# Kernel tuning notes

Hardware: AMD Instinct MI355X
Metric: run time of the kernel (lower is better)

## Reference

```python
import jax, jax.numpy as jnp
import numpy as np

N_NODES = 100000
N_EDGES = 1600000
IN_DIM = 128
HID = 128


def sage_conv(x, src, dst, W_l, W_r, b, num_nodes):
    # PyG SAGEConv (mean aggregation): out = lin_l(mean_{j in N(i)} x_j) + lin_r(x_i)
    msgs = x[src]                                            # [E, F] gather
    agg = jax.ops.segment_sum(msgs, dst, num_segments=num_nodes)  # [N, F]
    cnt = jax.ops.segment_sum(jnp.ones((src.shape[0],), x.dtype), dst,
                              num_segments=num_nodes)        # [N]
    agg = agg / jnp.maximum(cnt, 1.0)[:, None]               # mean; 0 for isolated nodes
    return agg @ W_l + b + x @ W_r


def setup_inputs() -> dict:
    key = jax.random.key(0)
    ks = jax.random.split(key, 12)
    s_in = 1.0 / np.sqrt(IN_DIM)
    s_h = 1.0 / np.sqrt(HID)
    return {
        "x": jax.random.normal(ks[0], (N_NODES, IN_DIM), jnp.float32),
        "edge_index": jax.random.randint(ks[1], (2, N_EDGES), 0, N_NODES, jnp.int64),
        "Wl1": jax.random.normal(ks[2], (IN_DIM, HID), jnp.float32) * s_in,
        "Wr1": jax.random.normal(ks[3], (IN_DIM, HID), jnp.float32) * s_in,
        "b1": jnp.zeros((HID,), jnp.float32),
        "Wl2": jax.random.normal(ks[4], (HID, HID), jnp.float32) * s_h,
        "Wr2": jax.random.normal(ks[5], (HID, HID), jnp.float32) * s_h,
        "b2": jnp.zeros((HID,), jnp.float32),
        "Wp": jax.random.normal(ks[6], (HID, 1), jnp.float32) * s_h,
        "bp": jnp.zeros((1,), jnp.float32),
        "Wd": jax.random.normal(ks[7], (HID, 1), jnp.float32) * s_h,
        "bd": jnp.zeros((1,), jnp.float32),
    }


def reference(x, edge_index, Wl1, Wr1, b1, Wl2, Wr2, b2, Wp, bp, Wd, bd):
    src, dst = edge_index[0], edge_index[1]
    h = jax.nn.relu(sage_conv(x, src, dst, Wl1, Wr1, b1, N_NODES))
    h = jax.nn.relu(sage_conv(h, src, dst, Wl2, Wr2, b2, N_NODES))
    preds = h @ Wp + bp                      # [N, 1]
    diffs = jax.nn.sigmoid(h @ Wd + bd)      # [N, 1]
    return (preds - diffs, preds + diffs)
```

## Files before the change

### kernel.cpp

```cpp
#include <hip/hip_runtime.h>
#include <hip/hip_bf16.h>

#define N_NODES 100000
#define N_EDGES 1600000
#define NBUCK 1563
#define BCAP 1216
#define PADC 1408
#define ACHUNK 4096
#define GTILES 1563
#define PABLK 391

typedef __bf16 bf16x8 __attribute__((ext_vector_type(8)));
typedef __bf16 bf16x4 __attribute__((ext_vector_type(4)));
typedef float  f32x4  __attribute__((ext_vector_type(4)));
typedef float  f32x2  __attribute__((ext_vector_type(2)));


#define ACC16(v)                                             \
  a01 += __builtin_amdgcn_cvt_pk_f32_fp8((v).x, false);      \
  a23 += __builtin_amdgcn_cvt_pk_f32_fp8((v).x, true);       \
  a45 += __builtin_amdgcn_cvt_pk_f32_fp8((v).y, false);      \
  a67 += __builtin_amdgcn_cvt_pk_f32_fp8((v).y, true);       \
  a89 += __builtin_amdgcn_cvt_pk_f32_fp8((v).z, false);      \
  aAB += __builtin_amdgcn_cvt_pk_f32_fp8((v).z, true);       \
  aCD += __builtin_amdgcn_cvt_pk_f32_fp8((v).w, false);      \
  aEF += __builtin_amdgcn_cvt_pk_f32_fp8((v).w, true);

#define WFRAG(ct, c) (*(const bf16x8*)&Wswz[(size_t)((((w * 4 + (ct)) * 4 + (c)) * 64) + lane) * 8])


__global__ __launch_bounds__(256) void init_kernel(int* __restrict__ bcnt,
                                                   int* __restrict__ P1s,
                                                   int* __restrict__ P2s,
                                                   const float* __restrict__ Wl1,
                                                   const float* __restrict__ Wr1,
                                                   const float* __restrict__ Wl2,
                                                   const float* __restrict__ Wr2,
                                                   __bf16* __restrict__ W1out,
                                                   __bf16* __restrict__ W2out) {
  const int b = blockIdx.x, t = threadIdx.x;
  if (b == 0) {
    for (int i = t; i < NBUCK; i += 256) bcnt[i] = 0;
    if (t < 32) { P1s[t] = 0; P2s[t] = 0; }
    return;
  }
  int gi = (b - 1) * 256 + t;
  bool L2 = gi >= 32768;
  int i = gi & 32767;
  int j = i & 7;
  int lane = (i >> 3) & 63;
  int c = (i >> 9) & 3;
  int tile = i >> 11;
  int k = c * 32 + ((lane >> 4) * 8) + j;
  int krow = L2 ? (((k & 7) << 4) | (k >> 3)) : k;
  int col = tile * 16 + (lane & 15);
  const float* Wl = L2 ? Wl2 : Wl1;
  const float* Wr = L2 ? Wr2 : Wr1;
  float v = (col < 128) ? Wl[krow * 128 + col] : Wr[krow * 128 + (col - 128)];
  (L2 ? W2out : W1out)[i] = (__bf16)v;
}


__global__ __launch_bounds__(256, 4) void work1_kernel(
    const float* __restrict__ A, const __bf16* __restrict__ Wswz,
    const float* __restrict__ bias, unsigned char* __restrict__ P,
    __bf16* __restrict__ R, int M,
    const int* __restrict__ src, const int* __restrict__ dst,
    int* __restrict__ bcnt, unsigned* __restrict__ packed, int E) {
  __shared__ __align__(16) char smem[64 * 144 * 2];
  const int t = threadIdx.x;

  if (blockIdx.x < PABLK) {
    int* hist = (int*)smem;
    int* curs = (int*)(smem + 6272);
    for (int i = t; i < NBUCK; i += 256) hist[i] = 0;
    __syncthreads();

    const int base = blockIdx.x * ACHUNK;
    const int lim = min(base + ACHUNK, E);

    int dloc[16], sloc[16];
    int myn = 0;
    for (int i = base + t; i < lim; i += 256) {
      dloc[myn] = dst[i];
      sloc[myn] = src[i];
      ++myn;
    }
    for (int k = 0; k < myn; ++k) atomicAdd(&hist[dloc[k] >> 6], 1);
    __syncthreads();

    for (int i = t; i < NBUCK; i += 256) {
      int h = hist[i];
      curs[i] = (h > 0) ? atomicAdd(&bcnt[i], h) : 0;
    }
    __syncthreads();

    for (int k = 0; k < myn; ++k) {
      int d = dloc[k];
      int b = d >> 6;
      int pos = atomicAdd(&curs[b], 1);
      if (pos < BCAP)
        packed[(size_t)b * BCAP + pos] = ((unsigned)sloc[k] << 6) | (unsigned)(d & 63);
    }
    return;
  }

  __bf16 (*ldsA)[144] = (__bf16 (*)[144])smem;
  const int lane = t & 63;
  const int w = t >> 6;
  const int q = lane >> 4;
  const int s = lane & 15;
  const int m0 = (blockIdx.x - PABLK) * 64;

#pragma unroll
  for (int it = 0; it < 8; ++it) {
    int row = it * 8 + (t >> 5);
    int col = (t & 31) * 4;
    float4 v = make_float4(0.f, 0.f, 0.f, 0.f);
    if (m0 + row < M) v = *(const float4*)&A[(size_t)(m0 + row) * 128 + col];
    bf16x4 bv;
    bv.x = (__bf16)v.x; bv.y = (__bf16)v.y; bv.z = (__bf16)v.z; bv.w = (__bf16)v.w;
    *(bf16x4*)&ldsA[row][col] = bv;
  }

  float breg[4];
#pragma unroll
  for (int j = 0; j < 4; ++j)
    breg[j] = (w >= 2) ? bias[((w - 2) * 4 + j) * 16 + s] : 0.f;

  __syncthreads();

#pragma unroll
  for (int half = 0; half < 2; ++half) {
    f32x4 acc[8];
    f32x4 zero = {0.f, 0.f, 0.f, 0.f};
#pragma unroll
    for (int i = 0; i < 8; ++i) acc[i] = zero;

    bf16x8 b0 = WFRAG(0, 0), b1 = WFRAG(1, 0), b2 = WFRAG(2, 0), b3 = WFRAG(3, 0);
#pragma unroll
    for (int c = 0; c < 4; ++c) {
      bf16x8 n0, n1, n2, n3;
      if (c < 3) { n0 = WFRAG(0, c + 1); n1 = WFRAG(1, c + 1); n2 = WFRAG(2, c + 1); n3 = WFRAG(3, c + 1); }
      bf16x8 a0 = *(const bf16x8*)&ldsA[(half * 2 + 0) * 16 + s][c * 32 + q * 8];
      bf16x8 a1 = *(const bf16x8*)&ldsA[(half * 2 + 1) * 16 + s][c * 32 + q * 8];
      acc[0] = __builtin_amdgcn_mfma_f32_16x16x32_bf16(a0, b0, acc[0], 0, 0, 0);
      acc[4] = __builtin_amdgcn_mfma_f32_16x16x32_bf16(a1, b0, acc[4], 0, 0, 0);
      acc[1] = __builtin_amdgcn_mfma_f32_16x16x32_bf16(a0, b1, acc[1], 0, 0, 0);
      acc[5] = __builtin_amdgcn_mfma_f32_16x16x32_bf16(a1, b1, acc[5], 0, 0, 0);
      acc[2] = __builtin_amdgcn_mfma_f32_16x16x32_bf16(a0, b2, acc[2], 0, 0, 0);
      acc[6] = __builtin_amdgcn_mfma_f32_16x16x32_bf16(a1, b2, acc[6], 0, 0, 0);
      acc[3] = __builtin_amdgcn_mfma_f32_16x16x32_bf16(a0, b3, acc[3], 0, 0, 0);
      acc[7] = __builtin_amdgcn_mfma_f32_16x16x32_bf16(a1, b3, acc[7], 0, 0, 0);
      if (c < 3) { b0 = n0; b1 = n1; b2 = n2; b3 = n3; }
    }

#pragma unroll
    for (int i = 0; i < 2; ++i) {
      int rt = half * 2 + i;
#pragma unroll
      for (int r = 0; r < 4; ++r) {
        int row = m0 + rt * 16 + q * 4 + r;
        if (row < M) {
          if (w < 2) {
            unsigned v = 0;
            v = __builtin_amdgcn_cvt_pk_fp8_f32(acc[i * 4 + 0][r], acc[i * 4 + 1][r], v, false);
            v = __builtin_amdgcn_cvt_pk_fp8_f32(acc[i * 4 + 2][r], acc[i * 4 + 3][r], v, true);
            *(unsigned*)&P[(size_t)row * 128 + s * 8 + w * 4] = v;
          } else {
            bf16x4 o;
#pragma unroll
            for (int ct = 0; ct < 4; ++ct) o[ct] = (__bf16)(acc[i * 4 + ct][r] + breg[ct]);
            *(bf16x4*)&R[(size_t)row * 128 + s * 8 + (w - 2) * 4] = o;
          }
        }
      }
    }
  }
}


__global__ __launch_bounds__(256, 4) void fusedB_kernel(
    const unsigned char* __restrict__ P1, __bf16* R,
    const unsigned* __restrict__ pck, const int* __restrict__ bcnt,
    const __bf16* __restrict__ Wswz, const float* __restrict__ bias,
    unsigned char* __restrict__ P2, int* __restrict__ srt,
    int* __restrict__ meta, int N) {
  __shared__ __bf16 Hlds[64][144];
  __shared__ int ssrcL[PADC];
  __shared__ int hist[64], pexcl[64], curs[64], scanb[64];
  __shared__ int gsteal;
  const int t = threadIdx.x;
  const int lane = t & 63;
  const int w = t >> 6;
  const int q = lane >> 4;
  const int s = lane & 15;
  const int b = blockIdx.x, nb = b * 64;

  if (t < 64) hist[t] = 0;
  if (t == 0) gsteal = 0;
  __syncthreads();

  const int ecnt = min(bcnt[b], BCAP);
  const unsigned* pk = pck + (size_t)b * BCAP;
  unsigned ploc[5];
  int myn = 0;
  for (int i = t; i < ecnt; i += 256) {
    unsigned p = pk[i];
    ploc[myn++] = p;
    atomicAdd(&hist[p & 63u], 1);
  }
  __syncthreads();

  int c0 = (t < 64) ? hist[t] : 0;
  int pc = (c0 + 3) & ~3;
  int x = pc;
  if (t < 64) scanb[t] = x;
  __syncthreads();
  for (int d = 1; d < 64; d <<= 1) {
    int y = (t >= d && t < 64) ? scanb[t - d] : 0;
    __syncthreads();
    if (t < 64) { x += y; scanb[t] = x; }
    __syncthreads();
  }
  if (t < 64) { pexcl[t] = x - pc; curs[t] = x - pc; }
  __syncthreads();

  for (int k = 0; k < myn; ++k) {
    unsigned p = ploc[k];
    int r = atomicAdd(&curs[p & 63u], 1);
    ssrcL[r] = (int)(p >> 6);
  }
  if (t < 64)
    for (int j = c0; j < pc; ++j) ssrcL[pexcl[t] + j] = N;
  __syncthreads();

  for (int i = t; i < PADC; i += 256) srt[(size_t)b * PADC + i] = ssrcL[i];
  if (t < 64) meta[b * 64 + t] = (pexcl[t] << 16) | hist[t];

  const int s8 = lane & 7;
  const int g8 = lane >> 3;
  const unsigned char* Pb = P1 + (size_t)s8 * 16;
  for (;;) {
    int n8;
    if (lane == 0) n8 = atomicAdd(&gsteal, 8);
    n8 = __shfl(n8, 0, 64);
    if (n8 >= 64) break;
    int dl = n8 + g8;
    int node = nb + dl;
    int start = pexcl[dl];
    int dg = hist[dl];
    int pend = start + ((dg + 3) & ~3);

    f32x2 a01 = {0.f, 0.f}, a23 = {0.f, 0.f}, a45 = {0.f, 0.f}, a67 = {0.f, 0.f};
    f32x2 a89 = {0.f, 0.f}, aAB = {0.f, 0.f}, aCD = {0.f, 0.f}, aEF = {0.f, 0.f};
    int cur = start;
    for (; cur + 8 <= pend; cur += 8) {
      int4 sv0 = *(const int4*)&ssrcL[cur];
      int4 sv1 = *(const int4*)&ssrcL[cur + 4];
      uint4 v0 = *(const uint4*)(Pb + (size_t)sv0.x * 128);
      uint4 v1 = *(const uint4*)(Pb + (size_t)sv0.y * 128);
      uint4 v2 = *(const uint4*)(Pb + (size_t)sv0.z * 128);
      uint4 v3 = *(const uint4*)(Pb + (size_t)sv0.w * 128);
      uint4 v4 = *(const uint4*)(Pb + (size_t)sv1.x * 128);
      uint4 v5 = *(const uint4*)(Pb + (size_t)sv1.y * 128);
      uint4 v6 = *(const uint4*)(Pb + (size_t)sv1.z * 128);
      uint4 v7 = *(const uint4*)(Pb + (size_t)sv1.w * 128);
      ACC16(v0) ACC16(v1) ACC16(v2) ACC16(v3)
      ACC16(v4) ACC16(v5) ACC16(v6) ACC16(v7)
    }
    if (cur < pend) {
      int4 sv = *(const int4*)&ssrcL[cur];
      uint4 v0 = *(const uint4*)(Pb + (size_t)sv.x * 128);
      uint4 v1 = *(const uint4*)(Pb + (size_t)sv.y * 128);
      uint4 v2 = *(const uint4*)(Pb + (size_t)sv.z * 128);
      uint4 v3 = *(const uint4*)(Pb + (size_t)sv.w * 128);
      ACC16(v0) ACC16(v1) ACC16(v2) ACC16(v3)
    }

    int nc = min(node, N - 1);
    float inv = 1.0f / (float)(dg > 0 ? dg : 1);
    const int p16 = s8 * 16;
    bf16x8 rv0 = *(const bf16x8*)&R[(size_t)nc * 128 + p16];
    bf16x8 rv1 = *(const bf16x8*)&R[(size_t)nc * 128 + p16 + 8];
    float ac[16] = {a01[0], a01[1], a23[0], a23[1], a45[0], a45[1], a67[0], a67[1],
                    a89[0], a89[1], aAB[0], aAB[1], aCD[0], aCD[1], aEF[0], aEF[1]};
    bf16x8 h0, h1;
#pragma unroll
    for (int j = 0; j < 8; ++j) {
      h0[j] = (__bf16)fmaxf(ac[j] * inv + (float)rv0[j], 0.f);
      h1[j] = (__bf16)fmaxf(ac[8 + j] * inv + (float)rv1[j], 0.f);
    }
    *(bf16x8*)&Hlds[dl][p16] = h0;
    *(bf16x8*)&Hlds[dl][p16 + 8] = h1;
  }
  __syncthreads();

  float breg[4];
#pragma unroll
  for (int j = 0; j < 4; ++j)
    breg[j] = (w >= 2) ? bias[((w - 2) * 4 + j) * 16 + s] : 0.f;

#pragma unroll
  for (int half = 0; half < 2; ++half) {
    f32x4 acc[8];
    f32x4 zero = {0.f, 0.f, 0.f, 0.f};
#pragma unroll
    for (int i = 0; i < 8; ++i) acc[i] = zero;

#pragma unroll
    for (int c = 0; c < 4; ++c) {
      bf16x8 a0 = *(const bf16x8*)&Hlds[(half * 2 + 0) * 16 + s][c * 32 + q * 8];
      bf16x8 a1 = *(const bf16x8*)&Hlds[(half * 2 + 1) * 16 + s][c * 32 + q * 8];
#pragma unroll
      for (int ct = 0; ct < 4; ++ct) {
        bf16x8 b = *(const bf16x8*)&Wswz[(size_t)((((w * 4 + ct) * 4 + c) * 64) + lane) * 8];
        acc[ct]     = __builtin_amdgcn_mfma_f32_16x16x32_bf16(a0, b, acc[ct], 0, 0, 0);
        acc[4 + ct] = __builtin_amdgcn_mfma_f32_16x16x32_bf16(a1, b, acc[4 + ct], 0, 0, 0);
      }
    }

#pragma unroll
    for (int i = 0; i < 2; ++i) {
      int rt = half * 2 + i;
#pragma unroll
      for (int r = 0; r < 4; ++r) {
        int row = nb + rt * 16 + q * 4 + r;
        if (row < N) {
          if (w < 2) {
            unsigned v = 0;
            v = __builtin_amdgcn_cvt_pk_fp8_f32(acc[i * 4 + 0][r], acc[i * 4 + 1][r], v, false);
            v = __builtin_amdgcn_cvt_pk_fp8_f32(acc[i * 4 + 2][r], acc[i * 4 + 3][r], v, true);
            *(unsigned*)&P2[(size_t)row * 128 + s * 8 + w * 4] = v;
          } else {
            bf16x4 o;
#pragma unroll
            for (int ct = 0; ct < 4; ++ct) o[ct] = (__bf16)(acc[i * 4 + ct][r] + breg[ct]);
            *(bf16x4*)&R[(size_t)row * 128 + s * 8 + (w - 2) * 4] = o;
          }
        }
      }
    }
  }
}


__global__ __launch_bounds__(256, 4) void fusedC_kernel(
    const unsigned char* __restrict__ P2, const __bf16* __restrict__ R,
    const int* __restrict__ srt, const int* __restrict__ meta,
    float* __restrict__ out,
    const float* __restrict__ Wp, const float* __restrict__ Wd,
    const float* __restrict__ bp, const float* __restrict__ bd, int N) {
  __shared__ int ssrcL[PADC];
  __shared__ int hist[64], pexcl[64];
  __shared__ int gsteal;
  const int t = threadIdx.x;
  const int lane = t & 63;
  const int b = blockIdx.x, nb = b * 64;

  for (int i = t; i < PADC; i += 256) ssrcL[i] = srt[(size_t)b * PADC + i];
  if (t < 64) {
    int m = meta[b * 64 + t];
    pexcl[t] = m >> 16;
    hist[t] = m & 0xffff;
  }
  if (t == 0) gsteal = 0;
  __syncthreads();

  const int s8 = lane & 7;
  const int g8 = lane >> 3;
  const unsigned char* Pb = P2 + (size_t)s8 * 16;
  for (;;) {
    int n8;
    if (lane == 0) n8 = atomicAdd(&gsteal, 8);
    n8 = __shfl(n8, 0, 64);
    if (n8 >= 64) break;
    int dl = n8 + g8;
    int node = nb + dl;
    int start = pexcl[dl];
    int dg = hist[dl];
    int pend = start + ((dg + 3) & ~3);

    f32x2 a01 = {0.f, 0.f}, a23 = {0.f, 0.f}, a45 = {0.f, 0.f}, a67 = {0.f, 0.f};
    f32x2 a89 = {0.f, 0.f}, aAB = {0.f, 0.f}, aCD = {0.f, 0.f}, aEF = {0.f, 0.f};
    int cur = start;
    for (; cur + 8 <= pend; cur += 8) {
      int4 sv0 = *(const int4*)&ssrcL[cur];
      int4 sv1 = *(const int4*)&ssrcL[cur + 4];
      uint4 v0 = *(const uint4*)(Pb + (size_t)sv0.x * 128);
      uint4 v1 = *(const uint4*)(Pb + (size_t)sv0.y * 128);
      uint4 v2 = *(const uint4*)(Pb + (size_t)sv0.z * 128);
      uint4 v3 = *(const uint4*)(Pb + (size_t)sv0.w * 128);
      uint4 v4 = *(const uint4*)(Pb + (size_t)sv1.x * 128);
      uint4 v5 = *(const uint4*)(Pb + (size_t)sv1.y * 128);
      uint4 v6 = *(const uint4*)(Pb + (size_t)sv1.z * 128);
      uint4 v7 = *(const uint4*)(Pb + (size_t)sv1.w * 128);
      ACC16(v0) ACC16(v1) ACC16(v2) ACC16(v3)
      ACC16(v4) ACC16(v5) ACC16(v6) ACC16(v7)
    }
    if (cur < pend) {
      int4 sv = *(const int4*)&ssrcL[cur];
      uint4 v0 = *(const uint4*)(Pb + (size_t)sv.x * 128);
      uint4 v1 = *(const uint4*)(Pb + (size_t)sv.y * 128);
      uint4 v2 = *(const uint4*)(Pb + (size_t)sv.z * 128);
      uint4 v3 = *(const uint4*)(Pb + (size_t)sv.w * 128);
      ACC16(v0) ACC16(v1) ACC16(v2) ACC16(v3)
    }

    int nc = min(node, N - 1);
    float inv = 1.0f / (float)(dg > 0 ? dg : 1);
    const int p16 = s8 * 16;
    bf16x8 rv0 = *(const bf16x8*)&R[(size_t)nc * 128 + p16];
    bf16x8 rv1 = *(const bf16x8*)&R[(size_t)nc * 128 + p16 + 8];
    float ac[16] = {a01[0], a01[1], a23[0], a23[1], a45[0], a45[1], a67[0], a67[1],
                    a89[0], a89[1], aAB[0], aAB[1], aCD[0], aCD[1], aEF[0], aEF[1]};
    float p = 0.f, dd = 0.f;
#pragma unroll
    for (int j = 0; j < 16; ++j) {
      int pos = p16 + j;
      int f = ((pos & 7) << 4) | (pos >> 3);
      float rvj = (float)((j < 8) ? rv0[j] : rv1[j - 8]);
      float h = fmaxf(ac[j] * inv + rvj, 0.f);
      p += h * Wp[f];
      dd += h * Wd[f];
    }
    p += __shfl_xor(p, 1, 64);  p += __shfl_xor(p, 2, 64);  p += __shfl_xor(p, 4, 64);
    dd += __shfl_xor(dd, 1, 64); dd += __shfl_xor(dd, 2, 64); dd += __shfl_xor(dd, 4, 64);
    if (node < N && s8 == 0) {
      float preds = p + bp[0];
      float sg = 1.0f / (1.0f + __expf(-(dd + bd[0])));
      out[node] = preds - sg;
      out[N + node] = preds + sg;
    }
  }
}


extern "C" void kernel_launch(void* const* d_in, const int* in_sizes, int n_in,
                              void* d_out, int out_size, void* d_ws, size_t ws_size,
                              hipStream_t stream) {
  const float* x    = (const float*)d_in[0];
  const int*   ei   = (const int*)d_in[1];
  const float* Wl1 = (const float*)d_in[2];
  const float* Wr1 = (const float*)d_in[3];
  const float* b1  = (const float*)d_in[4];
  const float* Wl2 = (const float*)d_in[5];
  const float* Wr2 = (const float*)d_in[6];
  const float* b2  = (const float*)d_in[7];
  const float* Wp  = (const float*)d_in[8];
  const float* bp  = (const float*)d_in[9];
  const float* Wd  = (const float*)d_in[10];
  const float* bd  = (const float*)d_in[11];
  float* out = (float*)d_out;

  const int N = N_NODES, E = N_EDGES;
  const int* src = ei;
  const int* dst = ei + E;

  char* w = (char*)d_ws;
  unsigned char* P1 = (unsigned char*)w; w += (size_t)(N + 1) * 128;
  unsigned char* P2 = (unsigned char*)w; w += (size_t)(N + 1) * 128;
  __bf16* Rbuf   = (__bf16*)w;   w += (size_t)N * 128 * 2;
  unsigned* pck  = (unsigned*)w; w += (size_t)NBUCK * BCAP * 4;
  int* bcnt      = (int*)w;      w += (size_t)(NBUCK + 32) * 4;
  __bf16* Ws1    = (__bf16*)w;   w += 65536;
  __bf16* Ws2    = (__bf16*)w;   w += 65536;
  int* srt       = (int*)w;      w += (size_t)NBUCK * PADC * 4;
  int* meta      = (int*)w;      w += (size_t)NBUCK * 64 * 4;

  init_kernel<<<257, 256, 0, stream>>>(bcnt,
                                       (int*)(P1 + (size_t)N * 128),
                                       (int*)(P2 + (size_t)N * 128),
                                       Wl1, Wr1, Wl2, Wr2, Ws1, Ws2);
  work1_kernel<<<GTILES + PABLK, 256, 0, stream>>>(x, Ws1, b1, P1, Rbuf, N,
                                                   src, dst, bcnt, pck, E);
  fusedB_kernel<<<NBUCK, 256, 0, stream>>>(P1, Rbuf, pck, bcnt, Ws2, b2, P2,
                                           srt, meta, N);
  fusedC_kernel<<<NBUCK, 256, 0, stream>>>(P2, Rbuf, srt, meta, out,
                                           Wp, Wd, bp, bd, N);
}
```

Baseline: 230.1 us.

## Split fused layer-2 gather+GEMM into separate gather and GEMM kernels

The fused layer-2 kernel is split in two. One kernel does the neighbour gather and mean, then writes the hidden activations to a global bf16 buffer. A second kernel loads 64-row tiles into LDS and runs the MFMA GEMM, software-prefetching the weight fragments one step ahead. The gather kernels drop the LDS tile and the 8-wide unrolled loop and raise launch_bounds occupancy to 6, so more waves can hide gather latency. The cost is an extra global write and read of the hidden activations (about 25 MB) plus one more kernel launch.

Result: slower. 243.3 us (+5.7%).

```diff
diff --git a/kernel.cpp b/kernel.cpp
--- a/kernel.cpp
+++ b/kernel.cpp
@@ -9,6 +9,7 @@
 #define ACHUNK 4096
 #define GTILES 1563
 #define PABLK 391
+#define HROWS (NBUCK * 64)
 
 typedef __bf16 bf16x8 __attribute__((ext_vector_type(8)));
 typedef __bf16 bf16x4 __attribute__((ext_vector_type(4)));
@@ -180,21 +181,16 @@
 }
 
 
-__global__ __launch_bounds__(256, 4) void fusedB_kernel(
-    const unsigned char* __restrict__ P1, __bf16* R,
+__global__ __launch_bounds__(256, 6) void gatherB_kernel(
+    const unsigned char* __restrict__ P1, const __bf16* __restrict__ R,
     const unsigned* __restrict__ pck, const int* __restrict__ bcnt,
-    const __bf16* __restrict__ Wswz, const float* __restrict__ bias,
-    unsigned char* __restrict__ P2, int* __restrict__ srt,
+    __bf16* __restrict__ H, int* __restrict__ srt,
     int* __restrict__ meta, int N) {
-  __shared__ __bf16 Hlds[64][144];
   __shared__ int ssrcL[PADC];
   __shared__ int hist[64], pexcl[64], curs[64], scanb[64];
   __shared__ int gsteal;
   const int t = threadIdx.x;
   const int lane = t & 63;
-  const int w = t >> 6;
-  const int q = lane >> 4;
-  const int s = lane & 15;
   const int b = blockIdx.x, nb = b * 64;
 
   if (t < 64) hist[t] = 0;
@@ -254,22 +250,7 @@
 
     f32x2 a01 = {0.f, 0.f}, a23 = {0.f, 0.f}, a45 = {0.f, 0.f}, a67 = {0.f, 0.f};
     f32x2 a89 = {0.f, 0.f}, aAB = {0.f, 0.f}, aCD = {0.f, 0.f}, aEF = {0.f, 0.f};
-    int cur = start;
-    for (; cur + 8 <= pend; cur += 8) {
-      int4 sv0 = *(const int4*)&ssrcL[cur];
-      int4 sv1 = *(const int4*)&ssrcL[cur + 4];
-      uint4 v0 = *(const uint4*)(Pb + (size_t)sv0.x * 128);
-      uint4 v1 = *(const uint4*)(Pb + (size_t)sv0.y * 128);
-      uint4 v2 = *(const uint4*)(Pb + (size_t)sv0.z * 128);
-      uint4 v3 = *(const uint4*)(Pb + (size_t)sv0.w * 128);
-      uint4 v4 = *(const uint4*)(Pb + (size_t)sv1.x * 128);
-      uint4 v5 = *(const uint4*)(Pb + (size_t)sv1.y * 128);
-      uint4 v6 = *(const uint4*)(Pb + (size_t)sv1.z * 128);
-      uint4 v7 = *(const uint4*)(Pb + (size_t)sv1.w * 128);
-      ACC16(v0) ACC16(v1) ACC16(v2) ACC16(v3)
-      ACC16(v4) ACC16(v5) ACC16(v6) ACC16(v7)
-    }
-    if (cur < pend) {
+    for (int cur = start; cur < pend; cur += 4) {
       int4 sv = *(const int4*)&ssrcL[cur];
       uint4 v0 = *(const uint4*)(Pb + (size_t)sv.x * 128);
       uint4 v1 = *(const uint4*)(Pb + (size_t)sv.y * 128);
@@ -291,15 +272,38 @@
       h0[j] = (__bf16)fmaxf(ac[j] * inv + (float)rv0[j], 0.f);
       h1[j] = (__bf16)fmaxf(ac[8 + j] * inv + (float)rv1[j], 0.f);
     }
-    *(bf16x8*)&Hlds[dl][p16] = h0;
-    *(bf16x8*)&Hlds[dl][p16 + 8] = h1;
-  }
-  __syncthreads();
+    *(bf16x8*)&H[(size_t)node * 128 + p16] = h0;
+    *(bf16x8*)&H[(size_t)node * 128 + p16 + 8] = h1;
+  }
+}
+
+
+__global__ __launch_bounds__(256, 4) void gemmB_kernel(
+    const __bf16* __restrict__ H, const __bf16* __restrict__ Wswz,
+    const float* __restrict__ bias, unsigned char* __restrict__ P2,
+    __bf16* __restrict__ R, int N) {
+  __shared__ __bf16 Hlds[64][144];
+  const int t = threadIdx.x;
+  const int lane = t & 63;
+  const int w = t >> 6;
+  const int q = lane >> 4;
+  const int s = lane & 15;
+  const int m0 = blockIdx.x * 64;
+
+#pragma unroll
+  for (int i = 0; i < 4; ++i) {
+    int row = i * 16 + (t >> 4);
+    int col = (t & 15) * 8;
+    bf16x8 v = *(const bf16x8*)&H[(size_t)(m0 + row) * 128 + col];
+    *(bf16x8*)&Hlds[row][col] = v;
+  }
 
   float breg[4];
 #pragma unroll
   for (int j = 0; j < 4; ++j)
     breg[j] = (w >= 2) ? bias[((w - 2) * 4 + j) * 16 + s] : 0.f;
+
+  __syncthreads();
 
 #pragma unroll
   for (int half = 0; half < 2; ++half) {
@@ -308,16 +312,22 @@
 #pragma unroll
     for (int i = 0; i < 8; ++i) acc[i] = zero;
 
+    bf16x8 b0 = WFRAG(0, 0), b1 = WFRAG(1, 0), b2 = WFRAG(2, 0), b3 = WFRAG(3, 0);
 #pragma unroll
     for (int c = 0; c < 4; ++c) {
+      bf16x8 n0, n1, n2, n3;
+      if (c < 3) { n0 = WFRAG(0, c + 1); n1 = WFRAG(1, c + 1); n2 = WFRAG(2, c + 1); n3 = WFRAG(3, c + 1); }
       bf16x8 a0 = *(const bf16x8*)&Hlds[(half * 2 + 0) * 16 + s][c * 32 + q * 8];
       bf16x8 a1 = *(const bf16x8*)&Hlds[(half * 2 + 1) * 16 + s][c * 32 + q * 8];
-#pragma unroll
-      for (int ct = 0; ct < 4; ++ct) {
-        bf16x8 b = *(const bf16x8*)&Wswz[(size_t)((((w * 4 + ct) * 4 + c) * 64) + lane) * 8];
-        acc[ct]     = __builtin_amdgcn_mfma_f32_16x16x32_bf16(a0, b, acc[ct], 0, 0, 0);
-        acc[4 + ct] = __builtin_amdgcn_mfma_f32_16x16x32_bf16(a1, b, acc[4 + ct], 0, 0, 0);
-      }
+      acc[0] = __builtin_amdgcn_mfma_f32_16x16x32_bf16(a0, b0, acc[0], 0, 0, 0);
+      acc[4] = __builtin_amdgcn_mfma_f32_16x16x32_bf16(a1, b0, acc[4], 0, 0, 0);
+      acc[1] = __builtin_amdgcn_mfma_f32_16x16x32_bf16(a0, b1, acc[1], 0, 0, 0);
+      acc[5] = __builtin_amdgcn_mfma_f32_16x16x32_bf16(a1, b1, acc[5], 0, 0, 0);
+      acc[2] = __builtin_amdgcn_mfma_f32_16x16x32_bf16(a0, b2, acc[2], 0, 0, 0);
+      acc[6] = __builtin_amdgcn_mfma_f32_16x16x32_bf16(a1, b2, acc[6], 0, 0, 0);
+      acc[3] = __builtin_amdgcn_mfma_f32_16x16x32_bf16(a0, b3, acc[3], 0, 0, 0);
+      acc[7] = __builtin_amdgcn_mfma_f32_16x16x32_bf16(a1, b3, acc[7], 0, 0, 0);
+      if (c < 3) { b0 = n0; b1 = n1; b2 = n2; b3 = n3; }
     }
 
 #pragma unroll
@@ -325,7 +335,7 @@
       int rt = half * 2 + i;
 #pragma unroll
       for (int r = 0; r < 4; ++r) {
-        int row = nb + rt * 16 + q * 4 + r;
+        int row = m0 + rt * 16 + q * 4 + r;
         if (row < N) {
           if (w < 2) {
             unsigned v = 0;
@@ -345,7 +355,7 @@
 }
 
 
-__global__ __launch_bounds__(256, 4) void fusedC_kernel(
+__global__ __launch_bounds__(256, 6) void fusedC_kernel(
     const unsigned char* __restrict__ P2, const __bf16* __restrict__ R,
     const int* __restrict__ srt, const int* __restrict__ meta,
     float* __restrict__ out,
@@ -383,22 +393,7 @@
 
     f32x2 a01 = {0.f, 0.f}, a23 = {0.f, 0.f}, a45 = {0.f, 0.f}, a67 = {0.f, 0.f};
     f32x2 a89 = {0.f, 0.f}, aAB = {0.f, 0.f}, aCD = {0.f, 0.f}, aEF = {0.f, 0.f};
-    int cur = start;
-    for (; cur + 8 <= pend; cur += 8) {
-      int4 sv0 = *(const int4*)&ssrcL[cur];
-      int4 sv1 = *(const int4*)&ssrcL[cur + 4];
-      uint4 v0 = *(const uint4*)(Pb + (size_t)sv0.x * 128);
-      uint4 v1 = *(const uint4*)(Pb + (size_t)sv0.y * 128);
-      uint4 v2 = *(const uint4*)(Pb + (size_t)sv0.z * 128);
-      uint4 v3 = *(const uint4*)(Pb + (size_t)sv0.w * 128);
-      uint4 v4 = *(const uint4*)(Pb + (size_t)sv1.x * 128);
-      uint4 v5 = *(const uint4*)(Pb + (size_t)sv1.y * 128);
-      uint4 v6 = *(const uint4*)(Pb + (size_t)sv1.z * 128);
-      uint4 v7 = *(const uint4*)(Pb + (size_t)sv1.w * 128);
-      ACC16(v0) ACC16(v1) ACC16(v2) ACC16(v3)
-      ACC16(v4) ACC16(v5) ACC16(v6) ACC16(v7)
-    }
-    if (cur < pend) {
+    for (int cur = start; cur < pend; cur += 4) {
       int4 sv = *(const int4*)&ssrcL[cur];
       uint4 v0 = *(const uint4*)(Pb + (size_t)sv.x * 128);
       uint4 v1 = *(const uint4*)(Pb + (size_t)sv.y * 128);
@@ -467,6 +462,7 @@
   __bf16* Ws2    = (__bf16*)w;   w += 65536;
   int* srt       = (int*)w;      w += (size_t)NBUCK * PADC * 4;
   int* meta      = (int*)w;      w += (size_t)NBUCK * 64 * 4;
+  __bf16* Hbuf   = (__bf16*)w;   w += (size_t)HROWS * 128 * 2;
 
   init_kernel<<<257, 256, 0, stream>>>(bcnt,
                                        (int*)(P1 + (size_t)N * 128),
@@ -474,8 +470,9 @@
                                        Wl1, Wr1, Wl2, Wr2, Ws1, Ws2);
   work1_kernel<<<GTILES + PABLK, 256, 0, stream>>>(x, Ws1, b1, P1, Rbuf, N,
                                                    src, dst, bcnt, pck, E);
-  fusedB_kernel<<<NBUCK, 256, 0, stream>>>(P1, Rbuf, pck, bcnt, Ws2, b2, P2,
-                                           srt, meta, N);
+  gatherB_kernel<<<NBUCK, 256, 0, stream>>>(P1, Rbuf, pck, bcnt, Hbuf,
+                                            srt, meta, N);
+  gemmB_kernel<<<GTILES, 256, 0, stream>>>(Hbuf, Ws2, b2, P2, Rbuf, N);
   fusedC_kernel<<<NBUCK, 256, 0, stream>>>(P2, Rbuf, srt, meta, out,
                                            Wp, Wd, bp, bd, N);
 }
```

## Fuse four kernels into persistent megakernel with software grid barriers

Applied to the files above, without the earlier changes.

Replaces the init, work1, fusedB and fusedC launches with one persistent kernel. Its grid is sized from the occupancy query (capped at 4 blocks per CU on 256 CUs), blocks loop over work units, and atomic spin grid barriers separate the phases. The aim is to remove launch gaps and tail drain between stages. It also simplifies the gather loops from 8-wide to 4-wide and drops the software prefetch of weight fragments. The risks are barrier spin overhead, possible deadlock if not all blocks are co-resident, and lower memory-level parallelism in the gather loops.

Result: slower. 760.3 us (+230.3%).

```diff
diff --git a/kernel.cpp b/kernel.cpp
--- a/kernel.cpp
+++ b/kernel.cpp
@@ -9,6 +9,7 @@
 #define ACHUNK 4096
 #define GTILES 1563
 #define PABLK 391
+#define WUNITS (GTILES + PABLK)
 
 typedef __bf16 bf16x8 __attribute__((ext_vector_type(8)));
 typedef __bf16 bf16x4 __attribute__((ext_vector_type(4)));
@@ -26,25 +27,35 @@
   aCD += __builtin_amdgcn_cvt_pk_f32_fp8((v).w, false);      \
   aEF += __builtin_amdgcn_cvt_pk_f32_fp8((v).w, true);
 
-#define WFRAG(ct, c) (*(const bf16x8*)&Wswz[(size_t)((((w * 4 + (ct)) * 4 + (c)) * 64) + lane) * 8])
-
-
-__global__ __launch_bounds__(256) void init_kernel(int* __restrict__ bcnt,
-                                                   int* __restrict__ P1s,
-                                                   int* __restrict__ P2s,
-                                                   const float* __restrict__ Wl1,
-                                                   const float* __restrict__ Wr1,
-                                                   const float* __restrict__ Wl2,
-                                                   const float* __restrict__ Wr2,
-                                                   __bf16* __restrict__ W1out,
-                                                   __bf16* __restrict__ W2out) {
-  const int b = blockIdx.x, t = threadIdx.x;
-  if (b == 0) {
+__device__ __forceinline__ bf16x8 wfrag(const __bf16* Wswz, int w, int lane, int ct, int c) {
+  return *(const bf16x8*)&Wswz[(size_t)((((w * 4 + ct) * 4 + c) * 64) + lane) * 8];
+}
+
+__device__ __forceinline__ void grid_barrier(int* bar, int target) {
+  __syncthreads();
+  if (threadIdx.x == 0) {
+    __threadfence();
+    __hip_atomic_fetch_add(bar, 1, __ATOMIC_ACQ_REL, __HIP_MEMORY_SCOPE_AGENT);
+    int spins = 0;
+    while (__hip_atomic_load(bar, __ATOMIC_ACQUIRE, __HIP_MEMORY_SCOPE_AGENT) < target) {
+      __builtin_amdgcn_s_sleep(32);
+      if (++spins > 4000000) break;
+    }
+    __threadfence();
+  }
+  __syncthreads();
+}
+
+
+__device__ __forceinline__ void dev_init(int u, int t, int* bcnt, int* P1s, int* P2s,
+    const float* Wl1, const float* Wr1, const float* Wl2, const float* Wr2,
+    __bf16* W1out, __bf16* W2out) {
+  if (u == 0) {
     for (int i = t; i < NBUCK; i += 256) bcnt[i] = 0;
     if (t < 32) { P1s[t] = 0; P2s[t] = 0; }
     return;
   }
-  int gi = (b - 1) * 256 + t;
+  int gi = (u - 1) * 256 + t;
   bool L2 = gi >= 32768;
   int i = gi & 32767;
   int j = i & 7;
@@ -61,24 +72,19 @@
 }
 
 
-__global__ __launch_bounds__(256, 4) void work1_kernel(
-    const float* __restrict__ A, const __bf16* __restrict__ Wswz,
-    const float* __restrict__ bias, unsigned char* __restrict__ P,
-    __bf16* __restrict__ R, int M,
-    const int* __restrict__ src, const int* __restrict__ dst,
-    int* __restrict__ bcnt, unsigned* __restrict__ packed, int E) {
-  __shared__ __align__(16) char smem[64 * 144 * 2];
-  const int t = threadIdx.x;
-
-  if (blockIdx.x < PABLK) {
+__device__ __forceinline__ void dev_work1(int u, int t, char* smem,
+    const float* A, const __bf16* Wswz, const float* bias,
+    unsigned char* P, __bf16* R, int M,
+    const int* src, const int* dst, int* bcnt, unsigned* packed, int E) {
+  __syncthreads();
+  if (u < PABLK) {
     int* hist = (int*)smem;
     int* curs = (int*)(smem + 6272);
     for (int i = t; i < NBUCK; i += 256) hist[i] = 0;
     __syncthreads();
 
-    const int base = blockIdx.x * ACHUNK;
+    const int base = u * ACHUNK;
     const int lim = min(base + ACHUNK, E);
-
     int dloc[16], sloc[16];
     int myn = 0;
     for (int i = base + t; i < lim; i += 256) {
@@ -110,7 +116,7 @@
   const int w = t >> 6;
   const int q = lane >> 4;
   const int s = lane & 15;
-  const int m0 = (blockIdx.x - PABLK) * 64;
+  const int m0 = (u - PABLK) * 64;
 
 #pragma unroll
   for (int it = 0; it < 8; ++it) {
@@ -137,22 +143,16 @@
 #pragma unroll
     for (int i = 0; i < 8; ++i) acc[i] = zero;
 
-    bf16x8 b0 = WFRAG(0, 0), b1 = WFRAG(1, 0), b2 = WFRAG(2, 0), b3 = WFRAG(3, 0);
 #pragma unroll
     for (int c = 0; c < 4; ++c) {
-      bf16x8 n0, n1, n2, n3;
-      if (c < 3) { n0 = WFRAG(0, c + 1); n1 = WFRAG(1, c + 1); n2 = WFRAG(2, c + 1); n3 = WFRAG(3, c + 1); }
       bf16x8 a0 = *(const bf16x8*)&ldsA[(half * 2 + 0) * 16 + s][c * 32 + q * 8];
       bf16x8 a1 = *(const bf16x8*)&ldsA[(half * 2 + 1) * 16 + s][c * 32 + q * 8];
-      acc[0] = __builtin_amdgcn_mfma_f32_16x16x32_bf16(a0, b0, acc[0], 0, 0, 0);
-      acc[4] = __builtin_amdgcn_mfma_f32_16x16x32_bf16(a1, b0, acc[4], 0, 0, 0);
-      acc[1] = __builtin_amdgcn_mfma_f32_16x16x32_bf16(a0, b1, acc[1], 0, 0, 0);
-      acc[5] = __builtin_amdgcn_mfma_f32_16x16x32_bf16(a1, b1, acc[5], 0, 0, 0);
-      acc[2] = __builtin_amdgcn_mfma_f32_16x16x32_bf16(a0, b2, acc[2], 0, 0, 0);
-      acc[6] = __builtin_amdgcn_mfma_f32_16x16x32_bf16(a1, b2, acc[6], 0, 0, 0);
-      acc[3] = __builtin_amdgcn_mfma_f32_16x16x32_bf16(a0, b3, acc[3], 0, 0, 0);
-      acc[7] = __builtin_amdgcn_mfma_f32_16x16x32_bf16(a1, b3, acc[7], 0, 0, 0);
-      if (c < 3) { b0 = n0; b1 = n1; b2 = n2; b3 = n3; }
+#pragma unroll
+      for (int ct = 0; ct < 4; ++ct) {
+        bf16x8 b = wfrag(Wswz, w, lane, ct, c);
+        acc[ct]     = __builtin_amdgcn_mfma_f32_16x16x32_bf16(a0, b, acc[ct], 0, 0, 0);
+        acc[4 + ct] = __builtin_amdgcn_mfma_f32_16x16x32_bf16(a1, b, acc[4 + ct], 0, 0, 0);
+      }
     }
 
 #pragma unroll
@@ -180,25 +180,26 @@
 }
 
 
-__global__ __launch_bounds__(256, 4) void fusedB_kernel(
-    const unsigned char* __restrict__ P1, __bf16* R,
-    const unsigned* __restrict__ pck, const int* __restrict__ bcnt,
-    const __bf16* __restrict__ Wswz, const float* __restrict__ bias,
-    unsigned char* __restrict__ P2, int* __restrict__ srt,
-    int* __restrict__ meta, int N) {
-  __shared__ __bf16 Hlds[64][144];
-  __shared__ int ssrcL[PADC];
-  __shared__ int hist[64], pexcl[64], curs[64], scanb[64];
-  __shared__ int gsteal;
-  const int t = threadIdx.x;
+__device__ __forceinline__ void dev_fusedB(int b, int t, char* smem,
+    const unsigned char* P1, __bf16* R, const unsigned* pck, const int* bcnt,
+    const __bf16* Wswz, const float* bias, unsigned char* P2,
+    int* srt, int* meta, int N) {
+  __bf16 (*Hlds)[144] = (__bf16 (*)[144])smem;
+  int* ssrcL = (int*)(smem + 18432);
+  int* hist  = (int*)(smem + 24064);
+  int* pexcl = (int*)(smem + 24320);
+  int* curs  = (int*)(smem + 24576);
+  int* scanb = (int*)(smem + 24832);
+  int* gst   = (int*)(smem + 25088);
   const int lane = t & 63;
   const int w = t >> 6;
   const int q = lane >> 4;
   const int s = lane & 15;
-  const int b = blockIdx.x, nb = b * 64;
-
+  const int nb = b * 64;
+
+  __syncthreads();
   if (t < 64) hist[t] = 0;
-  if (t == 0) gsteal = 0;
+  if (t == 0) *gst = 0;
   __syncthreads();
 
   const int ecnt = min(bcnt[b], BCAP);
@@ -243,7 +244,7 @@
   const unsigned char* Pb = P1 + (size_t)s8 * 16;
   for (;;) {
     int n8;
-    if (lane == 0) n8 = atomicAdd(&gsteal, 8);
+    if (lane == 0) n8 = atomicAdd(gst, 8);
     n8 = __shfl(n8, 0, 64);
     if (n8 >= 64) break;
     int dl = n8 + g8;
@@ -254,22 +255,7 @@
 
     f32x2 a01 = {0.f, 0.f}, a23 = {0.f, 0.f}, a45 = {0.f, 0.f}, a67 = {0.f, 0.f};
     f32x2 a89 = {0.f, 0.f}, aAB = {0.f, 0.f}, aCD = {0.f, 0.f}, aEF = {0.f, 0.f};
-    int cur = start;
-    for (; cur + 8 <= pend; cur += 8) {
-      int4 sv0 = *(const int4*)&ssrcL[cur];
-      int4 sv1 = *(const int4*)&ssrcL[cur + 4];
-      uint4 v0 = *(const uint4*)(Pb + (size_t)sv0.x * 128);
-      uint4 v1 = *(const uint4*)(Pb + (size_t)sv0.y * 128);
-      uint4 v2 = *(const uint4*)(Pb + (size_t)sv0.z * 128);
-      uint4 v3 = *(const uint4*)(Pb + (size_t)sv0.w * 128);
-      uint4 v4 = *(const uint4*)(Pb + (size_t)sv1.x * 128);
-      uint4 v5 = *(const uint4*)(Pb + (size_t)sv1.y * 128);
-      uint4 v6 = *(const uint4*)(Pb + (size_t)sv1.z * 128);
-      uint4 v7 = *(const uint4*)(Pb + (size_t)sv1.w * 128);
-      ACC16(v0) ACC16(v1) ACC16(v2) ACC16(v3)
-      ACC16(v4) ACC16(v5) ACC16(v6) ACC16(v7)
-    }
-    if (cur < pend) {
+    for (int cur = start; cur < pend; cur += 4) {
       int4 sv = *(const int4*)&ssrcL[cur];
       uint4 v0 = *(const uint4*)(Pb + (size_t)sv.x * 128);
       uint4 v1 = *(const uint4*)(Pb + (size_t)sv.y * 128);
@@ -314,9 +300,9 @@
       bf16x8 a1 = *(const bf16x8*)&Hlds[(half * 2 + 1) * 16 + s][c * 32 + q * 8];
 #pragma unroll
       for (int ct = 0; ct < 4; ++ct) {
-        bf16x8 b = *(const bf16x8*)&Wswz[(size_t)((((w * 4 + ct) * 4 + c) * 64) + lane) * 8];
-        acc[ct]     = __builtin_amdgcn_mfma_f32_16x16x32_bf16(a0, b, acc[ct], 0, 0, 0);
-        acc[4 + ct] = __builtin_amdgcn_mfma_f32_16x16x32_bf16(a1, b, acc[4 + ct], 0, 0, 0);
+        bf16x8 bb = wfrag(Wswz, w, lane, ct, c);
+        acc[ct]     = __builtin_amdgcn_mfma_f32_16x16x32_bf16(a0, bb, acc[ct], 0, 0, 0);
+        acc[4 + ct] = __builtin_amdgcn_mfma_f32_16x16x32_bf16(a1, bb, acc[4 + ct], 0, 0, 0);
       }
     }
 
@@ -345,26 +331,25 @@
 }
 
 
-__global__ __launch_bounds__(256, 4) void fusedC_kernel(
-    const unsigned char* __restrict__ P2, const __bf16* __restrict__ R,
-    const int* __restrict__ srt, const int* __restrict__ meta,
-    float* __restrict__ out,
-    const float* __restrict__ Wp, const float* __restrict__ Wd,
-    const float* __restrict__ bp, const float* __restrict__ bd, int N) {
-  __shared__ int ssrcL[PADC];
-  __shared__ int hist[64], pexcl[64];
-  __shared__ int gsteal;
-  const int t = threadIdx.x;
+__device__ __forceinline__ void dev_fusedC(int b, int t, char* smem,
+    const unsigned char* P2, const __bf16* R, const int* srt, const int* meta,
+    float* out, const float* Wp, const float* Wd,
+    const float* bp, const float* bd, int N) {
+  int* ssrcL = (int*)smem;
+  int* hist  = (int*)(smem + 5632);
+  int* pexcl = (int*)(smem + 5888);
+  int* gst   = (int*)(smem + 6144);
   const int lane = t & 63;
-  const int b = blockIdx.x, nb = b * 64;
-
+  const int nb = b * 64;
+
+  __syncthreads();
   for (int i = t; i < PADC; i += 256) ssrcL[i] = srt[(size_t)b * PADC + i];
   if (t < 64) {
     int m = meta[b * 64 + t];
     pexcl[t] = m >> 16;
     hist[t] = m & 0xffff;
   }
-  if (t == 0) gsteal = 0;
+  if (t == 0) *gst = 0;
   __syncthreads();
 
   const int s8 = lane & 7;
@@ -372,7 +357,7 @@
   const unsigned char* Pb = P2 + (size_t)s8 * 16;
   for (;;) {
     int n8;
-    if (lane == 0) n8 = atomicAdd(&gsteal, 8);
+    if (lane == 0) n8 = atomicAdd(gst, 8);
     n8 = __shfl(n8, 0, 64);
     if (n8 >= 64) break;
     int dl = n8 + g8;
@@ -383,22 +368,7 @@
 
     f32x2 a01 = {0.f, 0.f}, a23 = {0.f, 0.f}, a45 = {0.f, 0.f}, a67 = {0.f, 0.f};
     f32x2 a89 = {0.f, 0.f}, aAB = {0.f, 0.f}, aCD = {0.f, 0.f}, aEF = {0.f, 0.f};
-    int cur = start;
-    for (; cur + 8 <= pend; cur += 8) {
-      int4 sv0 = *(const int4*)&ssrcL[cur];
-      int4 sv1 = *(const int4*)&ssrcL[cur + 4];
-      uint4 v0 = *(const uint4*)(Pb + (size_t)sv0.x * 128);
-      uint4 v1 = *(const uint4*)(Pb + (size_t)sv0.y * 128);
-      uint4 v2 = *(const uint4*)(Pb + (size_t)sv0.z * 128);
-      uint4 v3 = *(const uint4*)(Pb + (size_t)sv0.w * 128);
-      uint4 v4 = *(const uint4*)(Pb + (size_t)sv1.x * 128);
-      uint4 v5 = *(const uint4*)(Pb + (size_t)sv1.y * 128);
-      uint4 v6 = *(const uint4*)(Pb + (size_t)sv1.z * 128);
-      uint4 v7 = *(const uint4*)(Pb + (size_t)sv1.w * 128);
-      ACC16(v0) ACC16(v1) ACC16(v2) ACC16(v3)
-      ACC16(v4) ACC16(v5) ACC16(v6) ACC16(v7)
-    }
-    if (cur < pend) {
+    for (int cur = start; cur < pend; cur += 4) {
       int4 sv = *(const int4*)&ssrcL[cur];
       uint4 v0 = *(const uint4*)(Pb + (size_t)sv.x * 128);
       uint4 v1 = *(const uint4*)(Pb + (size_t)sv.y * 128);
@@ -433,6 +403,40 @@
       out[N + node] = preds + sg;
     }
   }
+}
+
+
+__global__ __launch_bounds__(256, 4) void mega_kernel(
+    int* __restrict__ bar,
+    const float* __restrict__ x, const int* __restrict__ src, const int* __restrict__ dst,
+    const float* __restrict__ Wl1, const float* __restrict__ Wr1, const float* __restrict__ b1,
+    const float* __restrict__ Wl2, const float* __restrict__ Wr2, const float* __restrict__ b2,
+    const float* __restrict__ Wp, const float* __restrict__ bp,
+    const float* __restrict__ Wd, const float* __restrict__ bd,
+    unsigned char* __restrict__ P1, unsigned char* __restrict__ P2, __bf16* __restrict__ Rbuf,
+    unsigned* __restrict__ pck, int* __restrict__ bcnt,
+    __bf16* __restrict__ Ws1, __bf16* __restrict__ Ws2,
+    int* __restrict__ srt, int* __restrict__ meta, float* __restrict__ out,
+    int N, int E) {
+  __shared__ __align__(16) char smem[25600];
+  const int t = threadIdx.x;
+  const int G = gridDim.x;
+
+  for (int u = blockIdx.x; u < 257; u += G)
+    dev_init(u, t, bcnt, (int*)(P1 + (size_t)N * 128), (int*)(P2 + (size_t)N * 128),
+             Wl1, Wr1, Wl2, Wr2, Ws1, Ws2);
+  grid_barrier(bar, 1 * G);
+
+  for (int u = blockIdx.x; u < WUNITS; u += G)
+    dev_work1(u, t, smem, x, Ws1, b1, P1, Rbuf, N, src, dst, bcnt, pck, E);
+  grid_barrier(bar, 2 * G);
+
+  for (int u = blockIdx.x; u < NBUCK; u += G)
+    dev_fusedB(u, t, smem, P1, Rbuf, pck, bcnt, Ws2, b2, P2, srt, meta, N);
+  grid_barrier(bar, 3 * G);
+
+  for (int u = blockIdx.x; u < NBUCK; u += G)
+    dev_fusedC(u, t, smem, P2, Rbuf, srt, meta, out, Wp, Wd, bp, bd, N);
 }
 
 
@@ -458,6 +462,7 @@
   const int* dst = ei + E;
 
   char* w = (char*)d_ws;
+  int* bar       = (int*)w;      w += 64;
   unsigned char* P1 = (unsigned char*)w; w += (size_t)(N + 1) * 128;
   unsigned char* P2 = (unsigned char*)w; w += (size_t)(N + 1) * 128;
   __bf16* Rbuf   = (__bf16*)w;   w += (size_t)N * 128 * 2;
@@ -468,14 +473,19 @@
   int* srt       = (int*)w;      w += (size_t)NBUCK * PADC * 4;
   int* meta      = (int*)w;      w += (size_t)NBUCK * 64 * 4;
 
-  init_kernel<<<257, 256, 0, stream>>>(bcnt,
-                                       (int*)(P1 + (size_t)N * 128),
-                                       (int*)(P2 + (size_t)N * 128),
-                                       Wl1, Wr1, Wl2, Wr2, Ws1, Ws2);
-  work1_kernel<<<GTILES + PABLK, 256, 0, stream>>>(x, Ws1, b1, P1, Rbuf, N,
-                                                   src, dst, bcnt, pck, E);
-  fusedB_kernel<<<NBUCK, 256, 0, stream>>>(P1, Rbuf, pck, bcnt, Ws2, b2, P2,
-                                           srt, meta, N);
-  fusedC_kernel<<<NBUCK, 256, 0, stream>>>(P2, Rbuf, srt, meta, out,
-                                           Wp, Wd, bp, bd, N);
-}
+  static int blocksPerCU = 0;
+  if (blocksPerCU == 0) {
+    int nb = 0;
+    if (hipOccupancyMaxActiveBlocksPerMultiprocessor(&nb, mega_kernel, 256, 0) != hipSuccess || nb < 1)
+      nb = 2;
+    blocksPerCU = nb > 4 ? 4 : nb;
+  }
+  const int grid = blocksPerCU * 256;
+
+  hipMemsetAsync(bar, 0, 64, stream);
+  mega_kernel<<<grid, 256, 0, stream>>>(bar, x, src, dst,
+                                        Wl1, Wr1, b1, Wl2, Wr2, b2,
+                                        Wp, bp, Wd, bd,
+                                        P1, P2, Rbuf, pck, bcnt, Ws1, Ws2,
+                                        srt, meta, out, N, E);
+}
```
